# Kernel optimization log

Hardware: AMD Instinct MI355X
Metric: run time of the kernel (lower is better)

The kernel has to match this reference:

```python
import jax, jax.numpy as jnp
import numpy as np

N_NODES = 100000
N_EDGES = 1600000
NUM_GRAPHS = 128
EPS = 1e-5


def setup_inputs() -> dict:
    key = jax.random.key(0)
    ks = jax.random.split(key, 8)
    x = jax.random.normal(ks[0], (N_NODES, 8), dtype=jnp.float32)
    edge_index = jax.random.randint(ks[1], (2, N_EDGES), 0, N_NODES, dtype=jnp.int64)
    batch = jnp.sort(jax.random.randint(ks[2], (N_NODES,), 0, NUM_GRAPHS, dtype=jnp.int64))
    W1_l = jax.random.normal(ks[3], (128, 8), dtype=jnp.float32) * 0.3
    b1 = jnp.zeros((128,), dtype=jnp.float32)
    W1_r = jax.random.normal(ks[4], (128, 8), dtype=jnp.float32) * 0.3
    g1 = jnp.ones((128,), dtype=jnp.float32)
    beta1 = jnp.zeros((128,), dtype=jnp.float32)
    W2_l = jax.random.normal(ks[5], (128, 128), dtype=jnp.float32) * 0.08
    b2 = jnp.zeros((128,), dtype=jnp.float32)
    W2_r = jax.random.normal(ks[6], (128, 128), dtype=jnp.float32) * 0.08
    g2 = jnp.ones((128,), dtype=jnp.float32)
    beta2 = jnp.zeros((128,), dtype=jnp.float32)
    return dict(x=x, edge_index=edge_index, batch=batch,
                W1_l=W1_l, b1=b1, W1_r=W1_r, g1=g1, beta1=beta1,
                W2_l=W2_l, b2=b2, W2_r=W2_r, g2=g2, beta2=beta2)


def _sage_conv(x, src, dst, W_l, b, W_r):
    # PyG SAGEConv: out = lin_l(mean_j x_j) + lin_r(x_i); lin_r has no bias
    msg = x[src]                                              # [E, F]
    agg = jax.ops.segment_sum(msg, dst, num_segments=N_NODES)
    deg = jax.ops.segment_sum(jnp.ones((src.shape[0],), x.dtype), dst,
                              num_segments=N_NODES)
    agg = agg / jnp.maximum(deg, 1.0)[:, None]                # mean aggregation
    return agg @ W_l.T + b + x @ W_r.T


def _batch_norm(h, gamma, beta):
    # training-mode BN over the node dimension
    mu = jnp.mean(h, axis=0)
    var = jnp.mean(jnp.square(h - mu), axis=0)
    return gamma * (h - mu) * jax.lax.rsqrt(var + EPS) + beta


def reference(x, edge_index, batch, W1_l, b1, W1_r, g1, beta1,
              W2_l, b2, W2_r, g2, beta2):
    src, dst = edge_index[0], edge_index[1]
    x1 = jax.nn.relu(_batch_norm(_sage_conv(x, src, dst, W1_l, b1, W1_r), g1, beta1))
    x2 = jax.nn.relu(_batch_norm(_sage_conv(x1, src, dst, W2_l, b2, W2_r), g2, beta2))
    h = x1 + x2  # dropout is identity in eval mode
    # global mean pool per graph
    s = jax.ops.segment_sum(h, batch, num_segments=NUM_GRAPHS)
    cnt = jax.ops.segment_sum(jnp.ones((h.shape[0],), h.dtype), batch,
                              num_segments=NUM_GRAPHS)
    return s / jnp.maximum(cnt, 1.0)[:, None]                 # [NUM_GRAPHS, 128]
```

## Files before the change

### kernel.cpp

```cpp
#include <hip/hip_runtime.h>
#include <cstdint>
#include <cstddef>

namespace {

constexpr int N_NODES = 100000;
constexpr int N_EDGES = 1600000;
constexpr int NUM_GRAPHS = 128;
constexpr int F = 128;
constexpr float BN_EPS = 1e-5f;

constexpr int W_BUCK = 512;
constexpr int NBUCK = (N_NODES + W_BUCK - 1) / W_BUCK;
constexpr int CB = 400;
constexpr int CHUNK = N_EDGES / CB;

typedef float f32x4 __attribute__((ext_vector_type(4)));
typedef float f32x2 __attribute__((ext_vector_type(2)));
typedef short s16x8 __attribute__((ext_vector_type(8)));
typedef unsigned char uchar;
union B8 { uint4 u; s16x8 s; };

__device__ inline ushort f2bf(float x) {
    uint u = __float_as_uint(x);
    u += 0x7fffu + ((u >> 16) & 1u);
    return (ushort)(u >> 16);
}
__device__ inline float bf2f(ushort s) { return __uint_as_float(((uint)s) << 16); }
__device__ inline uint pack2(float lo, float hi) {
    return (uint)f2bf(lo) | ((uint)f2bf(hi) << 16);
}
__device__ inline float bflo(uint u) { return __uint_as_float(u << 16); }
__device__ inline float bfhi(uint u) { return __uint_as_float(u & 0xffff0000u); }

__device__ inline void acc4f8(float* a, uint u) {
    f32x2 lo = __builtin_amdgcn_cvt_pk_f32_fp8((int)u, false);
    f32x2 hi = __builtin_amdgcn_cvt_pk_f32_fp8((int)u, true);
    a[0] += lo[0]; a[1] += lo[1]; a[2] += hi[0]; a[3] += hi[1];
}


__global__ void __launch_bounds__(256) k_histA(const int* __restrict__ ei,
                                               int* __restrict__ gcount) {
    __shared__ int bins[NBUCK];
    int t = threadIdx.x;
    for (int i = t; i < NBUCK; i += 256) bins[i] = 0;
    __syncthreads();
    int e0 = blockIdx.x * CHUNK;
    for (int i = t; i < CHUNK; i += 256)
        atomicAdd(&bins[ei[N_EDGES + e0 + i] >> 9], 1);
    __syncthreads();
    for (int i = t; i < NBUCK; i += 256) gcount[i * CB + blockIdx.x] = bins[i];
}

__global__ void __launch_bounds__(512) k_scanA(int* __restrict__ g,
                                               int* __restrict__ bsum) {
    __shared__ int tmp[512];
    int b = blockIdx.x, t = threadIdx.x;
    int v = (t < CB) ? g[b * CB + t] : 0;
    tmp[t] = v;
    __syncthreads();
    #pragma unroll
    for (int d = 1; d < 512; d <<= 1) {
        int u = (t >= d) ? tmp[t - d] : 0;
        __syncthreads();
        tmp[t] += u;
        __syncthreads();
    }
    if (t < CB) g[b * CB + t] = tmp[t] - v;
    if (t == 511) bsum[b] = tmp[511];
}

__global__ void __launch_bounds__(256) k_scanB(int* __restrict__ bsum) {
    __shared__ int tmp[256];
    int t = threadIdx.x;
    int v = (t < NBUCK) ? bsum[t] : 0;
    tmp[t] = v;
    __syncthreads();
    #pragma unroll
    for (int d = 1; d < 256; d <<= 1) {
        int u = (t >= d) ? tmp[t - d] : 0;
        __syncthreads();
        tmp[t] += u;
        __syncthreads();
    }
    if (t < NBUCK) bsum[t] = tmp[t] - v;
}

__global__ void __launch_bounds__(256) k_part(const int* __restrict__ ei,
                                              const int* __restrict__ gloc,
                                              const int* __restrict__ bsum,
                                              uint* __restrict__ epk) {
    __shared__ int cur[NBUCK];
    int t = threadIdx.x;
    for (int i = t; i < NBUCK; i += 256)
        cur[i] = gloc[i * CB + blockIdx.x] + bsum[i];
    __syncthreads();
    int e0 = blockIdx.x * CHUNK;
    for (int i = t; i < CHUNK; i += 256) {
        int d = ei[N_EDGES + e0 + i];
        int s = ei[e0 + i];
        int p = atomicAdd(&cur[d >> 9], 1);
        epk[p] = ((uint)s << 9) | (uint)(d & 511);
    }
}

__global__ void __launch_bounds__(512) k_rank(const uint* __restrict__ epk,
                                              const int* __restrict__ bsum,
                                              int* __restrict__ offs,
                                              int* __restrict__ ssrc) {
    __shared__ int dcnt[W_BUCK];
    __shared__ int tmp[W_BUCK];
    __shared__ int cur[W_BUCK];
    int b = blockIdx.x, t = threadIdx.x;
    dcnt[t] = 0;
    __syncthreads();
    int s0 = bsum[b];
    int s1 = (b + 1 < NBUCK) ? bsum[b + 1] : N_EDGES;
    for (int i = s0 + t; i < s1; i += 512)
        atomicAdd(&dcnt[epk[i] & 511u], 1);
    __syncthreads();
    int v = dcnt[t];
    tmp[t] = v;
    __syncthreads();
    #pragma unroll
    for (int d = 1; d < 512; d <<= 1) {
        int u = (t >= d) ? tmp[t - d] : 0;
        __syncthreads();
        tmp[t] += u;
        __syncthreads();
    }
    int start = s0 + tmp[t] - v;
    int node = b * W_BUCK + t;
    if (node <= N_NODES) offs[node] = start;
    cur[t] = start;
    __syncthreads();
    for (int i = s0 + t; i < s1; i += 512) {
        uint u = epk[i];
        int p = atomicAdd(&cur[u & 511u], 1);
        ssrc[p] = (int)(u >> 9);
    }
}


__global__ void k_bound(const int* __restrict__ batch, int* __restrict__ gstart) {
    int i = blockIdx.x * 256 + threadIdx.x;
    if (i >= N_NODES) return;
    int b = batch[i];
    if (i == 0) {
        for (int g = 0; g <= b; ++g) gstart[g] = 0;
    } else {
        int p = batch[i - 1];
        if (p != b) for (int g = p + 1; g <= b; ++g) gstart[g] = i;
    }
    if (i == N_NODES - 1) {
        for (int g = b + 1; g <= NUM_GRAPHS; ++g) gstart[g] = N_NODES;
    }
}


__global__ void k_packbf(const float* __restrict__ Wl, const float* __restrict__ Wr,
                         ushort* __restrict__ Wcat) {
    int i = blockIdx.x * 256 + threadIdx.x;
    int f = i >> 7, k = i & 127;
    Wcat[f * 256 + k]       = f2bf(Wl[i]);
    Wcat[f * 256 + 128 + k] = f2bf(Wr[i]);
}

__global__ void k_packbf1(const float* __restrict__ W1l, const float* __restrict__ W1r,
                          ushort* __restrict__ Wcat1) {
    int i = blockIdx.x * 256 + threadIdx.x;
    int f = i >> 5, k = i & 31;
    float v = (k < 8) ? W1r[f * 8 + k] : ((k < 16) ? W1l[f * 8 + (k - 8)] : 0.f);
    Wcat1[i] = f2bf(v);
}


__global__ void k_agg1(const float* __restrict__ x, const int* __restrict__ offs,
                       const int* __restrict__ ssrc, ushort* __restrict__ xa) {
    int n = blockIdx.x * 256 + threadIdx.x;
    if (n >= N_NODES) return;
    int s0 = offs[n], s1 = offs[n + 1];
    float a0=0,a1=0,a2=0,a3=0,a4=0,a5=0,a6=0,a7=0;
    int j = s0;
    for (; j + 3 < s1; j += 4) {
        int sa = ssrc[j], sb = ssrc[j+1], sc = ssrc[j+2], sd = ssrc[j+3];
        const float4* pa = (const float4*)(x + (size_t)sa * 8);
        const float4* pb = (const float4*)(x + (size_t)sb * 8);
        const float4* pc = (const float4*)(x + (size_t)sc * 8);
        const float4* pd = (const float4*)(x + (size_t)sd * 8);
        float4 va0 = pa[0], va1 = pa[1], vb0 = pb[0], vb1 = pb[1];
        float4 vc0 = pc[0], vc1 = pc[1], vd0 = pd[0], vd1 = pd[1];
        a0 += (va0.x + vb0.x) + (vc0.x + vd0.x);
        a1 += (va0.y + vb0.y) + (vc0.y + vd0.y);
        a2 += (va0.z + vb0.z) + (vc0.z + vd0.z);
        a3 += (va0.w + vb0.w) + (vc0.w + vd0.w);
        a4 += (va1.x + vb1.x) + (vc1.x + vd1.x);
        a5 += (va1.y + vb1.y) + (vc1.y + vd1.y);
        a6 += (va1.z + vb1.z) + (vc1.z + vd1.z);
        a7 += (va1.w + vb1.w) + (vc1.w + vd1.w);
    }
    for (; j < s1; ++j) {
        const float4* xp = (const float4*)(x + (size_t)ssrc[j] * 8);
        float4 b0 = xp[0], b1 = xp[1];
        a0+=b0.x; a1+=b0.y; a2+=b0.z; a3+=b0.w;
        a4+=b1.x; a5+=b1.y; a6+=b1.z; a7+=b1.w;
    }
    int dg = s1 - s0;
    float inv = 1.0f / (float)(dg > 1 ? dg : 1);
    const float4* xp = (const float4*)(x + (size_t)n * 8);
    float4 x0 = xp[0], x1v = xp[1];
    ushort* row = xa + (size_t)n * 32;
    uint4 o0 = {pack2(x0.x, x0.y), pack2(x0.z, x0.w), pack2(x1v.x, x1v.y), pack2(x1v.z, x1v.w)};
    uint4 o1 = {pack2(a0*inv, a1*inv), pack2(a2*inv, a3*inv),
                pack2(a4*inv, a5*inv), pack2(a6*inv, a7*inv)};
    uint4 z = {0u, 0u, 0u, 0u};
    *(uint4*)(row)      = o0;
    *(uint4*)(row + 8)  = o1;
    *(uint4*)(row + 16) = z;
    *(uint4*)(row + 24) = z;
}

__global__ void __launch_bounds__(256) k_lin1(
        const ushort* __restrict__ xa, const ushort* __restrict__ Wcat1,
        const float* __restrict__ b1, ushort* __restrict__ h1bf,
        float* __restrict__ stats) {
    __shared__ ushort sOut[64 * 140];
    __shared__ float sred[256];
    int tid = threadIdx.x;
    int wave = tid >> 6, lane = tid & 63;
    int quad = lane >> 4, l16 = lane & 15;
    int n0 = blockIdx.x * 64;

    int node = n0 + wave * 16 + l16;
    int cn = (node < N_NODES) ? node : N_NODES - 1;
    B8 ta;
    ta.u = *(const uint4*)(xa + (size_t)cn * 32 + quad * 8);

    #pragma unroll
    for (int nt = 0; nt < 8; ++nt) {
        int fb = nt * 16 + l16;
        B8 tb;
        tb.u = *(const uint4*)(Wcat1 + fb * 32 + quad * 8);
        f32x4 acc = {0.f, 0.f, 0.f, 0.f};
        acc = __builtin_amdgcn_mfma_f32_16x16x32_bf16(ta.s, tb.s, acc, 0, 0, 0);
        float bb = b1[fb];
        #pragma unroll
        for (int r = 0; r < 4; ++r) {
            int row = wave * 16 + quad * 4 + r;
            sOut[row * 140 + fb] = f2bf(acc[r] + bb);
        }
    }
    __syncthreads();

    #pragma unroll
    for (int p = 0; p < 4; ++p) {
        int row = p * 16 + (tid >> 4);
        int nd = n0 + row;
        if (nd < N_NODES) {
            int c0 = (tid & 15) * 8;
            uint4 v = *(const uint4*)&sOut[row * 140 + c0];
            *(uint4*)(h1bf + (size_t)nd * F + c0) = v;
        }
    }

    int f = tid & 127, half = tid >> 7;
    float s = 0.f, s2 = 0.f;
    for (int r = half * 32; r < half * 32 + 32; ++r) {
        if (n0 + r >= N_NODES) break;
        float v = bf2f(sOut[r * 140 + f]);
        s += v; s2 += v * v;
    }
    if (half) { sred[f] = s; sred[128 + f] = s2; }
    __syncthreads();
    if (!half) {
        s += sred[f]; s2 += sred[128 + f];
        atomicAdd(&stats[f], s);
        atomicAdd(&stats[F + f], s2);
    }
}

__global__ void k_bnfin(const float* __restrict__ stats, const float* __restrict__ gamma,
                        const float* __restrict__ beta, float* __restrict__ scsh) {
    int f = threadIdx.x;
    float mu  = stats[f] * (1.0f / N_NODES);
    float var = stats[F + f] * (1.0f / N_NODES) - mu * mu;
    float sc  = gamma[f] * rsqrtf(var + BN_EPS);
    scsh[f] = sc;
    scsh[F + f] = beta[f] - mu * sc;
}

__global__ void k_bnrelu(const ushort* __restrict__ h, const float* __restrict__ scsh,
                         ushort* __restrict__ x1bf, uchar* __restrict__ x1f8) {
    int i = blockIdx.x * 256 + threadIdx.x;
    int base = i * 8;
    int f = base & (F - 1);
    float4 sc0 = *(const float4*)(scsh + f);
    float4 sc1 = *(const float4*)(scsh + f + 4);
    float4 sh0 = *(const float4*)(scsh + F + f);
    float4 sh1 = *(const float4*)(scsh + F + f + 4);
    uint4 hv = *(const uint4*)(h + base);
    float v0 = fmaxf(0.f, bflo(hv.x)*sc0.x + sh0.x);
    float v1 = fmaxf(0.f, bfhi(hv.x)*sc0.y + sh0.y);
    float v2 = fmaxf(0.f, bflo(hv.y)*sc0.z + sh0.z);
    float v3 = fmaxf(0.f, bfhi(hv.y)*sc0.w + sh0.w);
    float v4 = fmaxf(0.f, bflo(hv.z)*sc1.x + sh1.x);
    float v5 = fmaxf(0.f, bfhi(hv.z)*sc1.y + sh1.y);
    float v6 = fmaxf(0.f, bflo(hv.w)*sc1.z + sh1.z);
    float v7 = fmaxf(0.f, bfhi(hv.w)*sc1.w + sh1.w);
    uint4 o = {pack2(v0,v1), pack2(v2,v3), pack2(v4,v5), pack2(v6,v7)};
    *(uint4*)(x1bf + base) = o;
    int p0 = __builtin_amdgcn_cvt_pk_fp8_f32(v0, v1, 0, false);
    p0     = __builtin_amdgcn_cvt_pk_fp8_f32(v2, v3, p0, true);
    int p1 = __builtin_amdgcn_cvt_pk_fp8_f32(v4, v5, 0, false);
    p1     = __builtin_amdgcn_cvt_pk_fp8_f32(v6, v7, p1, true);
    uint2 o8 = {(uint)p0, (uint)p1};
    *(uint2*)(x1f8 + base) = o8;
}


__global__ void __launch_bounds__(256) k_agg2(
        const uchar* __restrict__ x1f8, const int* __restrict__ offs,
        const int* __restrict__ ssrc, ushort* __restrict__ agg2bf) {
    int t = threadIdx.x;
    int n = blockIdx.x * 32 + (t >> 3);
    int c16 = (t & 7) * 16;
    int s0 = offs[n], s1 = offs[n + 1];
    float acc[16];
    #pragma unroll
    for (int i = 0; i < 16; ++i) acc[i] = 0.f;
    int j = s0;
    for (; j + 3 < s1; j += 4) {
        int sa = ssrc[j], sb = ssrc[j+1], sc = ssrc[j+2], sd = ssrc[j+3];
        uint4 va = *(const uint4*)(x1f8 + (size_t)sa * F + c16);
        uint4 vb = *(const uint4*)(x1f8 + (size_t)sb * F + c16);
        uint4 vc = *(const uint4*)(x1f8 + (size_t)sc * F + c16);
        uint4 vd = *(const uint4*)(x1f8 + (size_t)sd * F + c16);
        acc4f8(acc,      va.x); acc4f8(acc + 4,  va.y);
        acc4f8(acc + 8,  va.z); acc4f8(acc + 12, va.w);
        acc4f8(acc,      vb.x); acc4f8(acc + 4,  vb.y);
        acc4f8(acc + 8,  vb.z); acc4f8(acc + 12, vb.w);
        acc4f8(acc,      vc.x); acc4f8(acc + 4,  vc.y);
        acc4f8(acc + 8,  vc.z); acc4f8(acc + 12, vc.w);
        acc4f8(acc,      vd.x); acc4f8(acc + 4,  vd.y);
        acc4f8(acc + 8,  vd.z); acc4f8(acc + 12, vd.w);
    }
    for (; j < s1; ++j) {
        uint4 v = *(const uint4*)(x1f8 + (size_t)ssrc[j] * F + c16);
        acc4f8(acc,      v.x); acc4f8(acc + 4,  v.y);
        acc4f8(acc + 8,  v.z); acc4f8(acc + 12, v.w);
    }
    int dg = s1 - s0;
    float inv = 1.0f / (float)(dg > 1 ? dg : 1);
    uint4 o0 = {pack2(acc[0]*inv,  acc[1]*inv),  pack2(acc[2]*inv,  acc[3]*inv),
                pack2(acc[4]*inv,  acc[5]*inv),  pack2(acc[6]*inv,  acc[7]*inv)};
    uint4 o1 = {pack2(acc[8]*inv,  acc[9]*inv),  pack2(acc[10]*inv, acc[11]*inv),
                pack2(acc[12]*inv, acc[13]*inv), pack2(acc[14]*inv, acc[15]*inv)};
    ushort* dst = agg2bf + (size_t)n * F + c16;
    *(uint4*)(dst)     = o0;
    *(uint4*)(dst + 8) = o1;
}

__global__ void __launch_bounds__(256, 2) k_lin2(
        const ushort* __restrict__ agg2bf, const ushort* __restrict__ x1bf,
        const ushort* __restrict__ Wcat, const float* __restrict__ b2,
        ushort* __restrict__ h2bf, float* __restrict__ stats) {
    __shared__ ushort sB[32 * 128 * 8];
    int tid = threadIdx.x;
    int wave = tid >> 6, lane = tid & 63;
    int quad = lane >> 4, l16 = lane & 15;
    int f0 = wave * 32 + l16;
    int f1 = f0 + 16;

    #pragma unroll
    for (int it = 0; it < 16; ++it) {
        int c = it * 256 + tid;
        int f = c >> 5, j = c & 31;
        uint4 v = *(const uint4*)(Wcat + (size_t)c * 8);
        *(uint4*)&sB[((j << 7) + f) * 8] = v;
    }
    __syncthreads();

    float bb0 = b2[f0], bb1 = b2[f1];
    float s0 = 0.f, s0q = 0.f, s1 = 0.f, s1q = 0.f;
    int n0 = blockIdx.x * 128;

    s16x8 aA[8], aB[8];
    auto loadA = [&](s16x8* a, int nb) {
        int an = nb + l16;
        if (an >= N_NODES) an = N_NODES - 1;
        #pragma unroll
        for (int ks = 0; ks < 8; ++ks) {
            const ushort* src = (ks < 4) ? agg2bf : x1bf;
            B8 tm;
            tm.u = *(const uint4*)(src + (size_t)an * F + (ks & 3) * 32 + quad * 8);
            a[ks] = tm.s;
        }
    };
    auto compute = [&](s16x8* a, int nb) {
        f32x4 acc0 = {0.f, 0.f, 0.f, 0.f};
        f32x4 acc1 = {0.f, 0.f, 0.f, 0.f};
        #pragma unroll
        for (int ks = 0; ks < 8; ++ks) {
            int j = (ks << 2) + quad;
            B8 tb0, tb1;
            tb0.u = *(const uint4*)&sB[((j << 7) + f0) * 8];
            tb1.u = *(const uint4*)&sB[((j << 7) + f1) * 8];
            acc0 = __builtin_amdgcn_mfma_f32_16x16x32_bf16(a[ks], tb0.s, acc0, 0, 0, 0);
            acc1 = __builtin_amdgcn_mfma_f32_16x16x32_bf16(a[ks], tb1.s, acc1, 0, 0, 0);
        }
        #pragma unroll
        for (int r = 0; r < 4; ++r) {
            int node = nb + quad * 4 + r;
            if (node < N_NODES) {
                float v0 = acc0[r] + bb0, v1 = acc1[r] + bb1;
                h2bf[(size_t)node * F + f0] = f2bf(v0);
                h2bf[(size_t)node * F + f1] = f2bf(v1);
                s0 += v0; s0q += v0 * v0;
                s1 += v1; s1q += v1 * v1;
            }
        }
    };

    loadA(aA, n0);
    #pragma unroll 1
    for (int p = 0; p < 4; ++p) {
        int nb = n0 + p * 32;
        loadA(aB, nb + 16);
        compute(aA, nb);
        if (p < 3) loadA(aA, nb + 32);
        compute(aB, nb + 16);
    }

    s0  += __shfl_xor(s0, 16);  s0  += __shfl_xor(s0, 32);
    s0q += __shfl_xor(s0q, 16); s0q += __shfl_xor(s0q, 32);
    s1  += __shfl_xor(s1, 16);  s1  += __shfl_xor(s1, 32);
    s1q += __shfl_xor(s1q, 16); s1q += __shfl_xor(s1q, 32);
    if (quad == 0) {
        atomicAdd(&stats[f0], s0);
        atomicAdd(&stats[F + f0], s0q);
        atomicAdd(&stats[f1], s1);
        atomicAdd(&stats[F + f1], s1q);
    }
}


__global__ void k_pool(const ushort* __restrict__ x1bf, const ushort* __restrict__ h2bf,
                       const float* __restrict__ scsh2, const int* __restrict__ batch,
                       float* __restrict__ outacc) {
    int f = threadIdx.x;
    int n0 = blockIdx.x * 128;
    int n1 = min(n0 + 128, N_NODES);
    float sc = scsh2[f], sh = scsh2[F + f];
    float acc = 0.f;
    int curg = batch[n0];
    for (int n = n0; n < n1; ++n) {
        int g = batch[n];
        if (g != curg) {
            atomicAdd(&outacc[curg * F + f], acc);
            acc = 0.f; curg = g;
        }
        float v1 = bf2f(x1bf[(size_t)n * F + f]);
        float v2 = fmaxf(0.f, bf2f(h2bf[(size_t)n * F + f]) * sc + sh);
        acc += v1 + v2;
    }
    atomicAdd(&outacc[curg * F + f], acc);
}

__global__ void k_out(const float* __restrict__ outacc, const int* __restrict__ gstart,
                      float* __restrict__ out) {
    int i = blockIdx.x * 256 + threadIdx.x;
    if (i >= NUM_GRAPHS * F) return;
    int g = i >> 7;
    int c = gstart[g + 1] - gstart[g];
    out[i] = outacc[i] / (float)(c > 1 ? c : 1);
}

}

extern "C" void kernel_launch(void* const* d_in, const int* in_sizes, int n_in,
                              void* d_out, int out_size, void* d_ws, size_t ws_size,
                              hipStream_t stream) {
    const float* x     = (const float*)d_in[0];
    const int*   ei    = (const int*)d_in[1];
    const int*   batch = (const int*)d_in[2];
    const float* W1l   = (const float*)d_in[3];
    const float* b1    = (const float*)d_in[4];
    const float* W1r   = (const float*)d_in[5];
    const float* g1    = (const float*)d_in[6];
    const float* be1   = (const float*)d_in[7];
    const float* W2l   = (const float*)d_in[8];
    const float* b2    = (const float*)d_in[9];
    const float* W2r   = (const float*)d_in[10];
    const float* g2    = (const float*)d_in[11];
    const float* be2   = (const float*)d_in[12];
    float* out = (float*)d_out;

    char* w = (char*)d_ws;
    size_t o = 0;
    auto alloc = [&](size_t bytes) {
        void* p = w + o;
        o += (bytes + 511) & ~(size_t)511;
        return p;
    };
    int*    offs   = (int*)alloc((size_t)(N_NODES + 1) * 4);
    int*    gcount = (int*)alloc((size_t)NBUCK * CB * 4);
    int*    bsum   = (int*)alloc((size_t)NBUCK * 4);
    int*    ssrc   = (int*)alloc((size_t)N_EDGES * 4);
    uint*   epk    = (uint*)alloc((size_t)N_EDGES * 4);
    int*    gstart = (int*)alloc((NUM_GRAPHS + 1) * 4);
    float*  stats  = (float*)alloc(512 * 4);
    float*  scsh   = (float*)alloc(512 * 4);
    ushort* Wcat   = (ushort*)alloc((size_t)F * 256 * 2);
    ushort* Wcat1  = (ushort*)alloc((size_t)F * 32 * 2);
    float*  outacc = (float*)alloc((size_t)NUM_GRAPHS * F * 4);
    ushort* xa     = (ushort*)alloc((size_t)N_NODES * 32 * 2);
    ushort* h1bf   = (ushort*)alloc((size_t)N_NODES * F * 2);
    ushort* x1bf   = (ushort*)alloc((size_t)N_NODES * F * 2);
    uchar*  x1f8   = (uchar*)alloc((size_t)N_NODES * F);
    ushort* agg2bf = (ushort*)alloc((size_t)N_NODES * F * 2);
    ushort* h2bf   = (ushort*)alloc((size_t)N_NODES * F * 2);

    hipMemsetAsync(stats,  0, 512 * 4, stream);
    hipMemsetAsync(outacc, 0, (size_t)NUM_GRAPHS * F * 4, stream);

    k_histA<<<CB, 256, 0, stream>>>(ei, gcount);
    k_scanA<<<NBUCK, 512, 0, stream>>>(gcount, bsum);
    k_scanB<<<1, 256, 0, stream>>>(bsum);
    k_part <<<CB, 256, 0, stream>>>(ei, gcount, bsum, epk);
    k_rank <<<NBUCK, 512, 0, stream>>>(epk, bsum, offs, ssrc);
    k_bound<<<(N_NODES + 255) / 256, 256, 0, stream>>>(batch, gstart);
    k_packbf <<<64, 256, 0, stream>>>(W2l, W2r, Wcat);
    k_packbf1<<<16, 256, 0, stream>>>(W1l, W1r, Wcat1);

    k_agg1  <<<(N_NODES + 255) / 256, 256, 0, stream>>>(x, offs, ssrc, xa);
    k_lin1  <<<(N_NODES + 63) / 64, 256, 0, stream>>>(xa, Wcat1, b1, h1bf, stats);
    k_bnfin <<<1, 128, 0, stream>>>(stats, g1, be1, scsh);
    k_bnrelu<<<(N_NODES * F / 8) / 256, 256, 0, stream>>>(h1bf, scsh, x1bf, x1f8);

    k_agg2  <<<N_NODES / 32, 256, 0, stream>>>(x1f8, offs, ssrc, agg2bf);
    k_lin2  <<<(N_NODES + 127) / 128, 256, 0, stream>>>(agg2bf, x1bf, Wcat, b2,
                                                        h2bf, stats + 256);
    k_bnfin <<<1, 128, 0, stream>>>(stats + 256, g2, be2, scsh + 256);

    k_pool<<<(N_NODES + 127) / 128, 128, 0, stream>>>(x1bf, h2bf, scsh + 256, batch, outacc);
    k_out <<<(NUM_GRAPHS * F + 255) / 256, 256, 0, stream>>>(outacc, gstart, out);
}
```

Baseline: 331.7 us.

## Restructure lin2 so each wave computes all features for its own node tile

k_lin2 now launches 512-thread blocks covering 256 nodes. Each wave loads its A fragments for 32 nodes once and loops over all 8 feature tiles, instead of four waves sharing nodes and splitting the features. Before, every wave reloaded the same A rows from global memory; now each row is read only once. Weight LDS layout is swizzled to avoid bank conflicts, and BN stats are reduced in shared memory before one atomic per feature per block. The trade-off is more registers per thread and the loss of the previous double-buffered load/compute overlap across iterations.

Result: slower. 432.8 us (+30.5%).

```diff
diff --git a/kernel.cpp b/kernel.cpp
--- a/kernel.cpp
+++ b/kernel.cpp
@@ -361,29 +361,34 @@
     *(uint4*)(dst + 8) = o1;
 }
 
-__global__ void __launch_bounds__(256, 2) k_lin2(
+__device__ inline int gSw(int f, int j) { return (f << 5) | ((j + f) & 31); }
+
+__global__ void __launch_bounds__(512, 4) k_lin2(
         const ushort* __restrict__ agg2bf, const ushort* __restrict__ x1bf,
         const ushort* __restrict__ Wcat, const float* __restrict__ b2,
         ushort* __restrict__ h2bf, float* __restrict__ stats) {
-    __shared__ ushort sB[32 * 128 * 8];
+    __shared__ ushort sB[4096 * 8];
     int tid = threadIdx.x;
     int wave = tid >> 6, lane = tid & 63;
     int quad = lane >> 4, l16 = lane & 15;
-    int f0 = wave * 32 + l16;
-    int f1 = f0 + 16;
-
-    #pragma unroll
-    for (int it = 0; it < 16; ++it) {
-        int c = it * 256 + tid;
+
+    #pragma unroll
+    for (int it = 0; it < 8; ++it) {
+        int c = it * 512 + tid;
         int f = c >> 5, j = c & 31;
         uint4 v = *(const uint4*)(Wcat + (size_t)c * 8);
-        *(uint4*)&sB[((j << 7) + f) * 8] = v;
-    }
-    __syncthreads();
-
-    float bb0 = b2[f0], bb1 = b2[f1];
-    float s0 = 0.f, s0q = 0.f, s1 = 0.f, s1q = 0.f;
-    int n0 = blockIdx.x * 128;
+        *(uint4*)&sB[gSw(f, j) * 8] = v;
+    }
+    float bb[8];
+    #pragma unroll
+    for (int ft = 0; ft < 8; ++ft) bb[ft] = b2[ft * 16 + l16];
+    __syncthreads();
+
+    float ss[8], sq[8];
+    #pragma unroll
+    for (int i = 0; i < 8; ++i) { ss[i] = 0.f; sq[i] = 0.f; }
+
+    int nbase = blockIdx.x * 256 + wave * 32;
 
     s16x8 aA[8], aB[8];
     auto loadA = [&](s16x8* a, int nb) {
@@ -398,49 +403,53 @@
         }
     };
     auto compute = [&](s16x8* a, int nb) {
-        f32x4 acc0 = {0.f, 0.f, 0.f, 0.f};
-        f32x4 acc1 = {0.f, 0.f, 0.f, 0.f};
         #pragma unroll
-        for (int ks = 0; ks < 8; ++ks) {
-            int j = (ks << 2) + quad;
-            B8 tb0, tb1;
-            tb0.u = *(const uint4*)&sB[((j << 7) + f0) * 8];
-            tb1.u = *(const uint4*)&sB[((j << 7) + f1) * 8];
-            acc0 = __builtin_amdgcn_mfma_f32_16x16x32_bf16(a[ks], tb0.s, acc0, 0, 0, 0);
-            acc1 = __builtin_amdgcn_mfma_f32_16x16x32_bf16(a[ks], tb1.s, acc1, 0, 0, 0);
-        }
-        #pragma unroll
-        for (int r = 0; r < 4; ++r) {
-            int node = nb + quad * 4 + r;
-            if (node < N_NODES) {
-                float v0 = acc0[r] + bb0, v1 = acc1[r] + bb1;
-                h2bf[(size_t)node * F + f0] = f2bf(v0);
-                h2bf[(size_t)node * F + f1] = f2bf(v1);
-                s0 += v0; s0q += v0 * v0;
-                s1 += v1; s1q += v1 * v1;
+        for (int ft = 0; ft < 8; ++ft) {
+            int f = ft * 16 + l16;
+            f32x4 acc = {0.f, 0.f, 0.f, 0.f};
+            #pragma unroll
+            for (int ks = 0; ks < 8; ++ks) {
+                B8 tb;
+                tb.u = *(const uint4*)&sB[gSw(f, (ks << 2) + quad) * 8];
+                acc = __builtin_amdgcn_mfma_f32_16x16x32_bf16(a[ks], tb.s, acc, 0, 0, 0);
+            }
+            #pragma unroll
+            for (int r = 0; r < 4; ++r) {
+                int node = nb + quad * 4 + r;
+                if (node < N_NODES) {
+                    float v = acc[r] + bb[ft];
+                    h2bf[(size_t)node * F + f] = f2bf(v);
+                    ss[ft] += v; sq[ft] += v * v;
+                }
             }
         }
     };
 
-    loadA(aA, n0);
-    #pragma unroll 1
-    for (int p = 0; p < 4; ++p) {
-        int nb = n0 + p * 32;
-        loadA(aB, nb + 16);
-        compute(aA, nb);
-        if (p < 3) loadA(aA, nb + 32);
-        compute(aB, nb + 16);
-    }
-
-    s0  += __shfl_xor(s0, 16);  s0  += __shfl_xor(s0, 32);
-    s0q += __shfl_xor(s0q, 16); s0q += __shfl_xor(s0q, 32);
-    s1  += __shfl_xor(s1, 16);  s1  += __shfl_xor(s1, 32);
-    s1q += __shfl_xor(s1q, 16); s1q += __shfl_xor(s1q, 32);
+    loadA(aA, nbase);
+    loadA(aB, nbase + 16);
+    compute(aA, nbase);
+    compute(aB, nbase + 16);
+
+    #pragma unroll
+    for (int i = 0; i < 8; ++i) {
+        ss[i] += __shfl_xor(ss[i], 16); ss[i] += __shfl_xor(ss[i], 32);
+        sq[i] += __shfl_xor(sq[i], 16); sq[i] += __shfl_xor(sq[i], 32);
+    }
+    __syncthreads();
+    float* sred = (float*)sB;
     if (quad == 0) {
-        atomicAdd(&stats[f0], s0);
-        atomicAdd(&stats[F + f0], s0q);
-        atomicAdd(&stats[f1], s1);
-        atomicAdd(&stats[F + f1], s1q);
+        #pragma unroll
+        for (int ft = 0; ft < 8; ++ft) {
+            sred[wave * 256 + ft * 16 + l16]       = ss[ft];
+            sred[wave * 256 + 128 + ft * 16 + l16] = sq[ft];
+        }
+    }
+    __syncthreads();
+    if (tid < 256) {
+        float s = 0.f;
+        #pragma unroll
+        for (int w2 = 0; w2 < 8; ++w2) s += sred[w2 * 256 + tid];
+        atomicAdd(&stats[tid], s);
     }
 }
 
@@ -539,7 +548,7 @@
     k_bnrelu<<<(N_NODES * F / 8) / 256, 256, 0, stream>>>(h1bf, scsh, x1bf, x1f8);
 
     k_agg2  <<<N_NODES / 32, 256, 0, stream>>>(x1f8, offs, ssrc, agg2bf);
-    k_lin2  <<<(N_NODES + 127) / 128, 256, 0, stream>>>(agg2bf, x1bf, Wcat, b2,
+    k_lin2  <<<(N_NODES + 255) / 256, 512, 0, stream>>>(agg2bf, x1bf, Wcat, b2,
                                                         h2bf, stats + 256);
     k_bnfin <<<1, 128, 0, stream>>>(stats + 256, g2, be2, scsh + 256);
 
```
